# Kernel tuning notes

Measured on AMD Instinct MI355X. Metric: run time of the kernel, lower is better.

## Reference

```python
import jax, jax.numpy as jnp
import numpy as np

KH, KW = 3, 3      # kernel_size
SH, SW = 1, 1      # stride
MINVAL, MAXVAL = -0.45, -0.15


def setup_inputs() -> dict:
    key = jax.random.key(0)
    kx, kw = jax.random.split(key)
    x = jax.random.normal(kx, (16, 128, 128, 16), dtype=jnp.float32)  # NHWC
    W = jax.random.uniform(kw, (KH, KW, 16, 32), minval=MINVAL, maxval=MAXVAL,
                           dtype=jnp.float32)  # [kh, kw, C_in, filters]
    return {"x": x, "W": W}


def _dilation(x, W):
    # Max-plus sliding-window 'convolution' (VALID padding):
    # out[b,i,j,f] = max_{di,dj,c} x[b, i*SH+di, j*SW+dj, c] + W[di,dj,c,f]
    kh, kw, C, F = W.shape
    B, H, Wd, _ = x.shape
    Hout = (H - kh) // SH + 1
    Wout = (Wd - kw) // SW + 1
    out = jnp.full((B, Hout, Wout, F), -jnp.inf, dtype=x.dtype)
    for di in range(kh):          # small fixed loop over kernel offsets
        for dj in range(kw):
            xs = x[:, di:di + Hout * SH:SH, dj:dj + Wout * SW:SW, :]  # [B,Hout,Wout,C]
            # add W for this offset, reduce max over input channels
            out = jnp.maximum(out, jnp.max(xs[..., :, None] + W[di, dj], axis=3))
    return out


def reference(x, W):
    # erosion(x) = -dilation(-x)
    return -_dilation(-x, W)
```

## Files before the change

kernel.cpp:

```cpp
#include <hip/hip_runtime.h>
#include <math.h>


#define TI 21
#define TROWS (TI + 2)
#define NCOL 8
#define SCOL 10
#define LROW 80
#define VCOL 68
#define VROW (NCOL * VCOL)

typedef _Float16 h2 __attribute__((ext_vector_type(2)));

__device__ __forceinline__ h2 hmin2(h2 a, h2 b) {
    return __builtin_elementwise_min(a, b);
}

__device__ __forceinline__ h2 pksub(h2 a, h2 b) {
    h2 d;
    asm("v_pk_add_f16 %0, %1, %2 neg_lo:[0,1] neg_hi:[0,1]"
        : "=v"(d) : "v"(a), "v"(b));
    return d;
}
__device__ __forceinline__ h2 pkmin(h2 a, h2 b) {
    h2 d;
    asm("v_pk_min_f16 %0, %1, %2" : "=v"(d) : "v"(a), "v"(b));
    return d;
}
__device__ __forceinline__ _Float16 minh(_Float16 a, _Float16 b) {
    _Float16 d;
    asm("v_min_f16 %0, %1, %2" : "=v"(d) : "v"(a), "v"(b));
    return d;
}

__device__ __forceinline__ h2 pkrtz(float a, float b) {
    auto r = __builtin_amdgcn_cvt_pkrtz(a, b);
    return *reinterpret_cast<h2*>(&r);
}

__device__ __forceinline__ h2 rowmin3(const float4* pr, const h2* w) {
    h2 t[12];
#pragma unroll
    for (int dj = 0; dj < 3; ++dj) {
        const h2* p = reinterpret_cast<const h2*>(&pr[dj]);
#pragma unroll
        for (int q = 0; q < 4; ++q)
            t[dj * 4 + q] = pksub(p[q], w[dj * 4 + q]);
    }
#pragma unroll
    for (int k = 0; k < 6; ++k) t[k] = pkmin(t[k], t[k + 6]);
    t[0] = pkmin(t[0], t[3]);
    t[1] = pkmin(t[1], t[4]);
    t[2] = pkmin(t[2], t[5]);
    return pkmin(pkmin(t[0], t[1]), t[2]);
}

__global__ __launch_bounds__(512)
__attribute__((amdgpu_waves_per_eu(4, 4)))
void erosion_kernel(
    const float* __restrict__ x, const float* __restrict__ Wt,
    float* __restrict__ out)
{
    __shared__ __align__(16) _Float16 tile[2 * TROWS * LROW];
    __shared__ __align__(16) _Float16 wbuf[2 * 2304];
    __shared__ __align__(16) _Float16 vm[TI * VROW];

    const int tid = threadIdx.x;
    const int f  = tid & 31;
    const int ch = (tid >> 5) & 1;
    const int jt = tid >> 6;
    const int b  = blockIdx.z;
    const int i0 = blockIdx.y * TI;
    const int jb = blockIdx.x * NCOL;

    if (tid < TROWS * 2 * SCOL) {
        const float* xg = x + (size_t)b * (128 * 128 * 16);
        int r   = tid / (2 * SCOL);
        int k   = tid % (2 * SCOL);
        int cc  = k >> 1;
        int ch2 = k & 1;
        int col = min(jb + cc, 127);
        const float* src = xg + ((size_t)(i0 + r) * 128 + col) * 16 + ch2 * 8;
        float4 lo = *reinterpret_cast<const float4*>(src);
        float4 hi = *reinterpret_cast<const float4*>(src + 4);
        h2 o[4] = { pkrtz(lo.x, lo.y), pkrtz(lo.z, lo.w),
                    pkrtz(hi.x, hi.y), pkrtz(hi.z, hi.w) };
        *reinterpret_cast<float4*>(
            &tile[ch2 * (TROWS * LROW) + r * LROW + cc * 8]) =
            *reinterpret_cast<float4*>(o);
    }

    {
        h2* wl = reinterpret_cast<h2*>(wbuf);
        auto wstage = [&](int t) {
            int g  = t >> 5;
            int ff = t & 31;
            int p  = g >> 3;
            int cp = g & 7;
            int ch2 = cp >> 2;
            int q  = cp & 3;
            wl[p * 256 + ch2 * 128 + ff * 4 + q] =
                pkrtz(Wt[g * 64 + ff], Wt[g * 64 + 32 + ff]);
        };
#pragma unroll
        for (int rr = 0; rr < 4; ++rr) wstage(rr * 512 + tid);
        if (tid < 2304 - 2048) wstage(2048 + tid);
    }

    __syncthreads();

    float4 w9[9];
    {
        unsigned wa = (unsigned)(uintptr_t)(&wbuf[0]) + ch * 512 + f * 16;
        asm volatile(
            "ds_read_b128 %0, %9 offset:0\n\t"
            "ds_read_b128 %1, %9 offset:1024\n\t"
            "ds_read_b128 %2, %9 offset:2048\n\t"
            "ds_read_b128 %3, %9 offset:3072\n\t"
            "ds_read_b128 %4, %9 offset:4096\n\t"
            "ds_read_b128 %5, %9 offset:5120\n\t"
            "ds_read_b128 %6, %9 offset:6144\n\t"
            "ds_read_b128 %7, %9 offset:7168\n\t"
            "ds_read_b128 %8, %9 offset:8192\n\t"
            "s_waitcnt lgkmcnt(0)"
            : "=&v"(w9[0]), "=&v"(w9[1]), "=&v"(w9[2]), "=&v"(w9[3]),
              "=&v"(w9[4]), "=&v"(w9[5]), "=&v"(w9[6]), "=&v"(w9[7]),
              "=&v"(w9[8])
            : "v"(wa)
            : "memory");
    }
    const h2* wh0 = reinterpret_cast<const h2*>(&w9[0]);
    const h2* wh1 = reinterpret_cast<const h2*>(&w9[3]);
    const h2* wh2 = reinterpret_cast<const h2*>(&w9[6]);

    const _Float16* lb = &tile[ch * (TROWS * LROW) + jt * 8];

    float4 preA[3], preB[3];
#pragma unroll
    for (int dj = 0; dj < 3; ++dj) {
        preA[dj] = *reinterpret_cast<const float4*>(lb + 0 * LROW + dj * 8);
        preB[dj] = *reinterpret_cast<const float4*>(lb + 1 * LROW + dj * 8);
    }

    const _Float16 HINF = (_Float16)__builtin_huge_valf();
    h2 accB = {HINF, HINF};
    h2 accC = {HINF, HINF};

    _Float16* vp = &vm[jt * VCOL + ch * 32 + f];

    {
        h2 n0 = rowmin3(preA, wh0);
        h2 n1 = rowmin3(preA, wh1);
        h2 n2 = rowmin3(preA, wh2);
        const _Float16* ln = lb + 2 * LROW;
#pragma unroll
        for (int dj = 0; dj < 3; ++dj)
            preA[dj] = *reinterpret_cast<const float4*>(ln + dj * 8);
        accC = pkmin(accB, n1);
        accB = n0;
        (void)n2;
    }
    {
        h2 n0 = rowmin3(preB, wh0);
        h2 n1 = rowmin3(preB, wh1);
        h2 n2 = rowmin3(preB, wh2);
        const _Float16* ln = lb + 3 * LROW;
#pragma unroll
        for (int dj = 0; dj < 3; ++dj)
            preB[dj] = *reinterpret_cast<const float4*>(ln + dj * 8);
        accC = pkmin(accB, n1);
        accB = n0;
        (void)n2;
    }

    const _Float16* ldp = lb + 4 * LROW;
#pragma clang loop unroll(disable)
    for (int it = 0; it < 10; ++it) {
        {
            h2 n0 = rowmin3(preA, wh0);
            h2 n1 = rowmin3(preA, wh1);
            h2 n2 = rowmin3(preA, wh2);
#pragma unroll
            for (int dj = 0; dj < 3; ++dj)
                preA[dj] = *reinterpret_cast<const float4*>(ldp + dj * 8);
            h2 fin2 = pkmin(accC, n2);
            accC = pkmin(accB, n1);
            accB = n0;
            vp[0] = minh(fin2[0], fin2[1]);
        }
        {
            h2 n0 = rowmin3(preB, wh0);
            h2 n1 = rowmin3(preB, wh1);
            h2 n2 = rowmin3(preB, wh2);
            const _Float16* ln = ldp + LROW;
#pragma unroll
            for (int dj = 0; dj < 3; ++dj)
                preB[dj] = *reinterpret_cast<const float4*>(ln + dj * 8);
            h2 fin2 = pkmin(accC, n2);
            accC = pkmin(accB, n1);
            accB = n0;
            vp[VROW] = minh(fin2[0], fin2[1]);
        }
        ldp += 2 * LROW;
        vp  += 2 * VROW;
    }

    {
        h2 n0 = rowmin3(preA, wh0);   (void)n0;
        h2 n1 = rowmin3(preA, wh1);   (void)n1;
        h2 n2 = rowmin3(preA, wh2);
        h2 fin2 = pkmin(accC, n2);
        vp[0] = minh(fin2[0], fin2[1]);
    }

    __syncthreads();

    {
        float* outb = out + (size_t)b * (126 * 126 * 32);
        auto merge = [&](int t) {
            int row = t >> 6;
            int k   = t & 63;
            int col = k >> 3;
            int q   = k & 7;
            int jj  = jb + col;
            const _Float16* base = &vm[row * VROW + col * VCOL + q * 4];
            h2 a[2], c[2];
            *reinterpret_cast<double*>(a) = *reinterpret_cast<const double*>(base);
            *reinterpret_cast<double*>(c) = *reinterpret_cast<const double*>(base + 32);
            h2 m0 = hmin2(a[0], c[0]);
            h2 m1 = hmin2(a[1], c[1]);
            float4 o = { (float)m0[0], (float)m0[1], (float)m1[0], (float)m1[1] };
            if (jj < 126)
                *reinterpret_cast<float4*>(
                    &outb[((size_t)(i0 + row) * 126 + jj) * 32 + q * 4]) = o;
        };
        merge(tid);
        merge(tid + 512);
        if (tid < TI * 64 - 1024) merge(tid + 1024);
    }
}

extern "C" void kernel_launch(void* const* d_in, const int* in_sizes, int n_in,
                              void* d_out, int out_size, void* d_ws, size_t ws_size,
                              hipStream_t stream) {
    const float* x  = (const float*)d_in[0];
    const float* Wt = (const float*)d_in[1];
    float* out = (float*)d_out;

    dim3 grid(16, 6, 16);
    dim3 block(512);
    erosion_kernel<<<grid, block, 0, stream>>>(x, Wt, out);
}
```

Before: 107.4 us.

## Process three row tiles per block with double-buffered input prefetch

Each block now handles three consecutive 21-row tiles instead of one, which cuts the grid to a third and reuses the weight staging across all three tiles. The next tile's input rows are fetched from global memory with inline asm loads while the current tile is computed, then written into a second LDS buffer after a barrier. This is meant to hide global load latency and amortise per-block setup. In exchange it adds LDS usage, extra barriers per tile, and leaves fewer blocks (512) to fill the GPU.

```diff
diff --git a/kernel.cpp b/kernel.cpp
--- a/kernel.cpp
+++ b/kernel.cpp
@@ -7,6 +7,7 @@
 #define NCOL 8
 #define SCOL 10
 #define LROW 80
+#define TSIZE (2 * TROWS * LROW)
 #define VCOL 68
 #define VROW (NCOL * VCOL)
 
@@ -32,7 +33,6 @@
     asm("v_min_f16 %0, %1, %2" : "=v"(d) : "v"(a), "v"(b));
     return d;
 }
-
 __device__ __forceinline__ h2 pkrtz(float a, float b) {
     auto r = __builtin_amdgcn_cvt_pkrtz(a, b);
     return *reinterpret_cast<h2*>(&r);
@@ -61,7 +61,7 @@
     const float* __restrict__ x, const float* __restrict__ Wt,
     float* __restrict__ out)
 {
-    __shared__ __align__(16) _Float16 tile[2 * TROWS * LROW];
+    __shared__ __align__(16) _Float16 tile2[2][TSIZE];
     __shared__ __align__(16) _Float16 wbuf[2 * 2304];
     __shared__ __align__(16) _Float16 vm[TI * VROW];
 
@@ -70,23 +70,25 @@
     const int ch = (tid >> 5) & 1;
     const int jt = tid >> 6;
     const int b  = blockIdx.z;
-    const int i0 = blockIdx.y * TI;
+    const int i0base = blockIdx.y * (3 * TI);
     const int jb = blockIdx.x * NCOL;
-
-    if (tid < TROWS * 2 * SCOL) {
-        const float* xg = x + (size_t)b * (128 * 128 * 16);
-        int r   = tid / (2 * SCOL);
-        int k   = tid % (2 * SCOL);
-        int cc  = k >> 1;
-        int ch2 = k & 1;
-        int col = min(jb + cc, 127);
-        const float* src = xg + ((size_t)(i0 + r) * 128 + col) * 16 + ch2 * 8;
+    const float* xg = x + (size_t)b * (128 * 128 * 16);
+
+    const bool stg = tid < TROWS * 2 * SCOL;
+    const int sr   = tid / (2 * SCOL);
+    const int sk   = tid % (2 * SCOL);
+    const int scc  = sk >> 1;
+    const int sch  = sk & 1;
+    const int scol = min(jb + scc, 127);
+    const int sdst = sch * (TROWS * LROW) + sr * LROW + scc * 8;
+
+    if (stg) {
+        const float* src = xg + ((size_t)(i0base + sr) * 128 + scol) * 16 + sch * 8;
         float4 lo = *reinterpret_cast<const float4*>(src);
         float4 hi = *reinterpret_cast<const float4*>(src + 4);
         h2 o[4] = { pkrtz(lo.x, lo.y), pkrtz(lo.z, lo.w),
                     pkrtz(hi.x, hi.y), pkrtz(hi.z, hi.w) };
-        *reinterpret_cast<float4*>(
-            &tile[ch2 * (TROWS * LROW) + r * LROW + cc * 8]) =
+        *reinterpret_cast<float4*>(&tile2[0][sdst]) =
             *reinterpret_cast<float4*>(o);
     }
 
@@ -133,110 +135,131 @@
     const h2* wh1 = reinterpret_cast<const h2*>(&w9[3]);
     const h2* wh2 = reinterpret_cast<const h2*>(&w9[6]);
 
-    const _Float16* lb = &tile[ch * (TROWS * LROW) + jt * 8];
-
-    float4 preA[3], preB[3];
-#pragma unroll
-    for (int dj = 0; dj < 3; ++dj) {
-        preA[dj] = *reinterpret_cast<const float4*>(lb + 0 * LROW + dj * 8);
-        preB[dj] = *reinterpret_cast<const float4*>(lb + 1 * LROW + dj * 8);
-    }
-
     const _Float16 HINF = (_Float16)__builtin_huge_valf();
-    h2 accB = {HINF, HINF};
-    h2 accC = {HINF, HINF};
-
-    _Float16* vp = &vm[jt * VCOL + ch * 32 + f];
-
-    {
-        h2 n0 = rowmin3(preA, wh0);
-        h2 n1 = rowmin3(preA, wh1);
-        h2 n2 = rowmin3(preA, wh2);
-        const _Float16* ln = lb + 2 * LROW;
-#pragma unroll
-        for (int dj = 0; dj < 3; ++dj)
-            preA[dj] = *reinterpret_cast<const float4*>(ln + dj * 8);
-        accC = pkmin(accB, n1);
-        accB = n0;
-        (void)n2;
-    }
-    {
-        h2 n0 = rowmin3(preB, wh0);
-        h2 n1 = rowmin3(preB, wh1);
-        h2 n2 = rowmin3(preB, wh2);
-        const _Float16* ln = lb + 3 * LROW;
-#pragma unroll
-        for (int dj = 0; dj < 3; ++dj)
-            preB[dj] = *reinterpret_cast<const float4*>(ln + dj * 8);
-        accC = pkmin(accB, n1);
-        accB = n0;
-        (void)n2;
-    }
-
-    const _Float16* ldp = lb + 4 * LROW;
-#pragma clang loop unroll(disable)
-    for (int it = 0; it < 10; ++it) {
+    float* outb = out + (size_t)b * (126 * 126 * 32);
+
+    for (int t = 0; t < 3; ++t) {
+        const _Float16* buf = tile2[t & 1];
+        const int i0 = i0base + t * TI;
+
+        float4 sl, sh;
+        const bool do_next = (t < 2) && stg;
+        if (do_next) {
+            const float* src =
+                xg + ((size_t)(i0 + TI + sr) * 128 + scol) * 16 + sch * 8;
+            asm volatile(
+                "global_load_dwordx4 %0, %2, off\n\t"
+                "global_load_dwordx4 %1, %2, off offset:16"
+                : "=&v"(sl), "=&v"(sh)
+                : "v"(src)
+                : "memory");
+        }
+
+        const _Float16* lb = buf + ch * (TROWS * LROW) + jt * 8;
+        float4 preA[3], preB[3];
+#pragma unroll
+        for (int dj = 0; dj < 3; ++dj) {
+            preA[dj] = *reinterpret_cast<const float4*>(lb + 0 * LROW + dj * 8);
+            preB[dj] = *reinterpret_cast<const float4*>(lb + 1 * LROW + dj * 8);
+        }
+        h2 accB = {HINF, HINF};
+        h2 accC = {HINF, HINF};
+        _Float16* vp = &vm[jt * VCOL + ch * 32 + f];
+
         {
             h2 n0 = rowmin3(preA, wh0);
             h2 n1 = rowmin3(preA, wh1);
-            h2 n2 = rowmin3(preA, wh2);
+            const _Float16* ln = lb + 2 * LROW;
 #pragma unroll
             for (int dj = 0; dj < 3; ++dj)
-                preA[dj] = *reinterpret_cast<const float4*>(ldp + dj * 8);
-            h2 fin2 = pkmin(accC, n2);
+                preA[dj] = *reinterpret_cast<const float4*>(ln + dj * 8);
             accC = pkmin(accB, n1);
             accB = n0;
-            vp[0] = minh(fin2[0], fin2[1]);
         }
         {
             h2 n0 = rowmin3(preB, wh0);
             h2 n1 = rowmin3(preB, wh1);
-            h2 n2 = rowmin3(preB, wh2);
-            const _Float16* ln = ldp + LROW;
+            const _Float16* ln = lb + 3 * LROW;
 #pragma unroll
             for (int dj = 0; dj < 3; ++dj)
                 preB[dj] = *reinterpret_cast<const float4*>(ln + dj * 8);
-            h2 fin2 = pkmin(accC, n2);
             accC = pkmin(accB, n1);
             accB = n0;
-            vp[VROW] = minh(fin2[0], fin2[1]);
-        }
-        ldp += 2 * LROW;
-        vp  += 2 * VROW;
-    }
-
-    {
-        h2 n0 = rowmin3(preA, wh0);   (void)n0;
-        h2 n1 = rowmin3(preA, wh1);   (void)n1;
-        h2 n2 = rowmin3(preA, wh2);
-        h2 fin2 = pkmin(accC, n2);
-        vp[0] = minh(fin2[0], fin2[1]);
-    }
-
-    __syncthreads();
-
-    {
-        float* outb = out + (size_t)b * (126 * 126 * 32);
-        auto merge = [&](int t) {
-            int row = t >> 6;
-            int k   = t & 63;
-            int col = k >> 3;
-            int q   = k & 7;
-            int jj  = jb + col;
-            const _Float16* base = &vm[row * VROW + col * VCOL + q * 4];
-            h2 a[2], c[2];
-            *reinterpret_cast<double*>(a) = *reinterpret_cast<const double*>(base);
-            *reinterpret_cast<double*>(c) = *reinterpret_cast<const double*>(base + 32);
-            h2 m0 = hmin2(a[0], c[0]);
-            h2 m1 = hmin2(a[1], c[1]);
-            float4 o = { (float)m0[0], (float)m0[1], (float)m1[0], (float)m1[1] };
-            if (jj < 126)
-                *reinterpret_cast<float4*>(
-                    &outb[((size_t)(i0 + row) * 126 + jj) * 32 + q * 4]) = o;
-        };
-        merge(tid);
-        merge(tid + 512);
-        if (tid < TI * 64 - 1024) merge(tid + 1024);
+        }
+        const _Float16* ldp = lb + 4 * LROW;
+#pragma clang loop unroll(disable)
+        for (int it = 0; it < 10; ++it) {
+            {
+                h2 n0 = rowmin3(preA, wh0);
+                h2 n1 = rowmin3(preA, wh1);
+                h2 n2 = rowmin3(preA, wh2);
+#pragma unroll
+                for (int dj = 0; dj < 3; ++dj)
+                    preA[dj] = *reinterpret_cast<const float4*>(ldp + dj * 8);
+                h2 fin2 = pkmin(accC, n2);
+                accC = pkmin(accB, n1);
+                accB = n0;
+                vp[0] = minh(fin2[0], fin2[1]);
+            }
+            {
+                h2 n0 = rowmin3(preB, wh0);
+                h2 n1 = rowmin3(preB, wh1);
+                h2 n2 = rowmin3(preB, wh2);
+                const _Float16* ln = ldp + LROW;
+#pragma unroll
+                for (int dj = 0; dj < 3; ++dj)
+                    preB[dj] = *reinterpret_cast<const float4*>(ln + dj * 8);
+                h2 fin2 = pkmin(accC, n2);
+                accC = pkmin(accB, n1);
+                accB = n0;
+                vp[VROW] = minh(fin2[0], fin2[1]);
+            }
+            ldp += 2 * LROW;
+            vp  += 2 * VROW;
+        }
+        {
+            h2 n2 = rowmin3(preA, wh2);
+            h2 fin2 = pkmin(accC, n2);
+            vp[0] = minh(fin2[0], fin2[1]);
+        }
+
+        __syncthreads();
+
+        if (do_next) {
+            asm volatile("s_waitcnt vmcnt(0)" ::: "memory");
+            h2 o[4] = { pkrtz(sl.x, sl.y), pkrtz(sl.z, sl.w),
+                        pkrtz(sh.x, sh.y), pkrtz(sh.z, sh.w) };
+            *reinterpret_cast<float4*>(&tile2[(t + 1) & 1][sdst]) =
+                *reinterpret_cast<float4*>(o);
+        }
+
+        {
+            auto merge = [&](int tt) {
+                int row = tt >> 6;
+                int k   = tt & 63;
+                int col = k >> 3;
+                int q   = k & 7;
+                int jj  = jb + col;
+                const _Float16* base = &vm[row * VROW + col * VCOL + q * 4];
+                h2 a[2], c[2];
+                *reinterpret_cast<double*>(a) =
+                    *reinterpret_cast<const double*>(base);
+                *reinterpret_cast<double*>(c) =
+                    *reinterpret_cast<const double*>(base + 32);
+                h2 m0 = hmin2(a[0], c[0]);
+                h2 m1 = hmin2(a[1], c[1]);
+                float4 o = { (float)m0[0], (float)m0[1],
+                             (float)m1[0], (float)m1[1] };
+                if (jj < 126)
+                    *reinterpret_cast<float4*>(
+                        &outb[((size_t)(i0 + row) * 126 + jj) * 32 + q * 4]) = o;
+            };
+            merge(tid);
+            merge(tid + 512);
+            if (tid < TI * 64 - 1024) merge(tid + 1024);
+        }
+
+        __syncthreads();
     }
 }
 
@@ -247,7 +270,7 @@
     const float* Wt = (const float*)d_in[1];
     float* out = (float*)d_out;
 
-    dim3 grid(16, 6, 16);
+    dim3 grid(16, 2, 16);
     dim3 block(512);
     erosion_kernel<<<grid, block, 0, stream>>>(x, Wt, out);
 }
```

Result: slower. 109.6 us (+2.1%).
